# Kernel tuning notes

Measured on AMD Instinct MI355X. Metric: run time of the kernel, lower is better.

Reference implementation:

```python
import jax, jax.numpy as jnp
import numpy as np

K_BINS = 8192
HIDDEN = 2048
SQRT2 = 1.4142135623730951
LEAKY_SLOPE = 0.01
TMIN = 1e-10


def setup_inputs() -> dict:
    key = jax.random.key(0)
    k0, k1, k2 = jax.random.split(key, 3)
    D = 2 * K_BINS  # mu length so that cat([mu, t]) has 2K+1 features
    # positive mu keeps mu ** (gamma - 1/(1-gamma)) (a fractional power) finite
    mu = jax.random.uniform(k0, (D,), jnp.float32, 0.1, 1.0)
    t = jnp.array([0.5], jnp.float32)
    gamma = jnp.array([0.5], jnp.float32)  # 1/(1-gamma) = 2 -> integral exponent
    W1 = jax.random.normal(k1, (D + 1, HIDDEN), jnp.float32) * (1.0 / np.sqrt(D + 1))
    b1 = jnp.zeros((HIDDEN,), jnp.float32)
    W2 = jax.random.normal(k2, (HIDDEN, D), jnp.float32) * (1.0 / np.sqrt(HIDDEN))
    b2 = jnp.zeros((D,), jnp.float32)
    return {"mu": mu, "t": t, "gamma": gamma, "W1": W1, "b1": b1,
            "W2": W2, "b2": b2, "K": K_BINS}


def reference(mu, t, gamma, W1, b1, W2, b2, K):
    g = gamma[0]
    # --- NN(cat([mu, t])) -> (mu_epsilon, ln_sigma_epsilon), each [K] ---
    inp = jnp.concatenate([mu, t])                      # [2K+1]
    h = jax.nn.leaky_relu(inp @ W1 + b1, LEAKY_SLOPE)   # [hidden]
    out = h @ W2 + b2                                   # [2K]
    mu_eps, ln_sig = out[:K], out[K:]
    # --- mu_x / sigma_x (t < tmin branch folded in via where) ---
    p_mu = g - 1.0 / (1.0 - g)
    p_eps = 1.0 / (1.0 - g)
    mu_x_nn = jnp.power(mu[:K], p_mu) * jnp.power(mu_eps, p_eps)
    sigma_x_nn = jnp.power(1.0 - g, -0.5) * jnp.exp(0.5 * ln_sig)
    use_nn = t[0] >= TMIN
    mu_x = jnp.where(use_nn, mu_x_nn, jnp.zeros_like(mu_eps))     # [K]
    sigma_x = jnp.where(use_nn, sigma_x_nn, jnp.ones_like(mu_eps))  # [K]
    # --- vectorized discretised CDF differences over the (D_out, K) grid ---
    kk = jnp.arange(K, dtype=jnp.float32)
    kl = 2.0 * (kk - 1.0) / (K - 1.0)   # left bin edges  [K]
    kr = 2.0 * kk / (K - 1.0)           # right bin edges [K]

    def cdf(x):  # x: [K] edges -> G: [D_out, K]
        z = (x[None, :] - mu_x[:, None]) / (sigma_x[:, None] * SQRT2)
        F = 0.5 * (1.0 + jax.lax.erf(z))
        return jnp.where(x[None, :] <= -1.0, 0.0,
                         jnp.where(x[None, :] >= 1.0, 1.0, F))

    return cdf(kr) - cdf(kl)  # [K, K] per-bin probabilities
```

## Files before the change

### kernel.cpp

```cpp
#include <hip/hip_runtime.h>
#include <math.h>

#define KBINS 8192
#define DDIM  16384
#define HID   2048
#define LASTROW 16384

#define C1 8
#define NCH1 2048
#define C2 8
#define NCH2 256

static constexpr float SQRT2_F  = 1.4142135623730951f;
static constexpr float INVSQ2PI = 0.3989422804014327f;

__device__ __forceinline__ float fast_erff(float x) {
    float ax = fabsf(x);
    float t  = 1.0f / fmaf(0.3275911f, ax, 1.0f);
    float p  = t * (0.254829592f +
               t * (-0.284496736f +
               t * (1.421413741f +
               t * (-1.453152027f +
               t * 1.061405429f))));
    float r = 1.0f - p * __expf(-ax * ax);
    return copysignf(r, x);
}

__global__ void __launch_bounds__(256)
mv1_partial(const float* __restrict__ mu, const float* __restrict__ W1,
            float* __restrict__ part1) {
    __shared__ float a_s[C1];
    int r0 = blockIdx.x * C1;
    if (threadIdx.x < C1) a_s[threadIdx.x] = mu[r0 + threadIdx.x];
    __syncthreads();
    int c0 = threadIdx.x * 4;
    const float* wp = W1 + (size_t)r0 * HID;
    float4 acc0 = {0.f, 0.f, 0.f, 0.f};
    float4 acc1 = {0.f, 0.f, 0.f, 0.f};
#pragma unroll
    for (int k = 0; k < C1; ++k) {
        float a = a_s[k];
        const float4 w0 = *reinterpret_cast<const float4*>(wp + (size_t)k * HID + c0);
        const float4 w1 = *reinterpret_cast<const float4*>(wp + (size_t)k * HID + c0 + 1024);
        acc0.x += a * w0.x; acc0.y += a * w0.y; acc0.z += a * w0.z; acc0.w += a * w0.w;
        acc1.x += a * w1.x; acc1.y += a * w1.y; acc1.z += a * w1.z; acc1.w += a * w1.w;
    }
    float* pp = part1 + (size_t)blockIdx.x * HID;
    *reinterpret_cast<float4*>(pp + c0)        = acc0;
    *reinterpret_cast<float4*>(pp + c0 + 1024) = acc1;
}

__global__ void __launch_bounds__(256)
h_reduce(const float* __restrict__ part1, const float* __restrict__ b1,
         const float* __restrict__ W1, const float* __restrict__ t,
         float* __restrict__ h) {
    __shared__ float red[16][17];
    int col_l = threadIdx.x & 15;
    int sub   = threadIdx.x >> 4;
    int c0    = blockIdx.x * 16;
    float s = 0.f;
    const float* p = part1 + c0 + col_l;
#pragma unroll 8
    for (int m = 0; m < 128; ++m)
        s += p[(size_t)(sub + (m << 4)) * HID];
    red[sub][col_l] = s;
    __syncthreads();
    if (threadIdx.x < 16) {
        int c = c0 + threadIdx.x;
        float v = b1[c] + t[0] * W1[(size_t)LASTROW * HID + c];
#pragma unroll
        for (int q = 0; q < 16; ++q) v += red[q][threadIdx.x];
        h[c] = (v >= 0.f) ? v : 0.01f * v;
    }
}

__global__ void __launch_bounds__(256)
mv2_partial(const float* __restrict__ h, const float* __restrict__ W2,
            float* __restrict__ part2) {
    __shared__ float hs[C2];
    int r0    = blockIdx.y * C2;
    int cbase = blockIdx.x * 2048;
    if (threadIdx.x < C2) hs[threadIdx.x] = h[r0 + threadIdx.x];
    __syncthreads();
    int c0 = cbase + threadIdx.x * 4;
    const float* wp = W2 + (size_t)r0 * DDIM;
    float4 acc0 = {0.f, 0.f, 0.f, 0.f};
    float4 acc1 = {0.f, 0.f, 0.f, 0.f};
#pragma unroll
    for (int k = 0; k < C2; ++k) {
        float a = hs[k];
        const float4 w0 = *reinterpret_cast<const float4*>(wp + (size_t)k * DDIM + c0);
        const float4 w1 = *reinterpret_cast<const float4*>(wp + (size_t)k * DDIM + c0 + 1024);
        acc0.x += a * w0.x; acc0.y += a * w0.y; acc0.z += a * w0.z; acc0.w += a * w0.w;
        acc1.x += a * w1.x; acc1.y += a * w1.y; acc1.z += a * w1.z; acc1.w += a * w1.w;
    }
    float* pp = part2 + (size_t)blockIdx.y * DDIM;
    *reinterpret_cast<float4*>(pp + c0)        = acc0;
    *reinterpret_cast<float4*>(pp + c0 + 1024) = acc1;
}

__global__ void __launch_bounds__(256)
scalars(const float* __restrict__ part2, const float* __restrict__ b2,
        const float* __restrict__ mu, const float* __restrict__ t,
        const float* __restrict__ gamma,
        float* __restrict__ mu_x, float* __restrict__ sigma_x) {
    __shared__ float red0[8][32];
    __shared__ float red1[8][32];
    int col_l = threadIdx.x & 31;
    int sub   = threadIdx.x >> 5;
    int c     = blockIdx.x * 32 + col_l;
    float s0 = 0.f, s1 = 0.f;
    const float* p0 = part2 + c;
    const float* p1 = part2 + c + KBINS;
#pragma unroll 8
    for (int m = 0; m < 32; ++m) {
        size_t off = (size_t)(sub + (m << 3)) * DDIM;
        s0 += p0[off];
        s1 += p1[off];
    }
    red0[sub][col_l] = s0;
    red1[sub][col_l] = s1;
    __syncthreads();
    if (threadIdx.x < 32) {
        int cc = blockIdx.x * 32 + threadIdx.x;
        float v0 = b2[cc];
        float v1 = b2[cc + KBINS];
#pragma unroll
        for (int p = 0; p < 8; ++p) { v0 += red0[p][threadIdx.x]; v1 += red1[p][threadIdx.x]; }
        float g  = gamma[0];
        float pe = 1.0f / (1.0f - g);
        float pm = g - pe;
        bool use_nn = (t[0] >= 1e-10f);
        float mx = powf(mu[cc], pm) * powf(v0, pe);
        float sx = powf(1.0f - g, -0.5f) * expf(0.5f * v1);
        mu_x[cc]    = use_nn ? mx : 0.0f;
        sigma_x[cc] = use_nn ? sx : 1.0f;
    }
}

__global__ void __launch_bounds__(256)
cdf_row(const float* __restrict__ mu_x, const float* __restrict__ sigma_x,
        float* __restrict__ out) {
    int tid = threadIdx.x;
    for (int rr = 0; rr < 2; ++rr) {
        int i = blockIdx.x * 2 + rr;
        float m    = mu_x[i];
        float invs = 1.0f / sigma_x[i];
        const float sc = 2.0f / 8191.0f;
        float A    = sc * invs;
        float B    = (-1.0f / 8191.0f - m) * invs;
        float coef = INVSQ2PI * A;
        float* orow = out + (size_t)i * KBINS;
#pragma unroll
        for (int it = 0; it < 8; ++it) {
            int j0 = it * 1024 + tid * 4;
            float4 r;
            if (j0 < 4096) {
                float u0 = fmaf((float)j0, A, B);
                float u1 = u0 + A;
                float u2 = u1 + A;
                float u3 = u2 + A;
                r.x = coef * __expf(-0.5f * u0 * u0);
                r.y = coef * __expf(-0.5f * u1 * u1);
                r.z = coef * __expf(-0.5f * u2 * u2);
                r.w = coef * __expf(-0.5f * u3 * u3);
            } else if (j0 == 4096) {
                float z = (8190.0f / 8191.0f - m) * invs * (1.0f / SQRT2_F);
                r.x = 0.5f * (1.0f - fast_erff(z));
                r.y = r.z = r.w = 0.f;
            } else {
                r.x = r.y = r.z = r.w = 0.f;
            }
            *reinterpret_cast<float4*>(orow + j0) = r;
        }
    }
}

extern "C" void kernel_launch(void* const* d_in, const int* in_sizes, int n_in,
                              void* d_out, int out_size, void* d_ws, size_t ws_size,
                              hipStream_t stream) {
    const float* mu    = (const float*)d_in[0];
    const float* t     = (const float*)d_in[1];
    const float* gamma = (const float*)d_in[2];
    const float* W1    = (const float*)d_in[3];
    const float* b1    = (const float*)d_in[4];
    const float* W2    = (const float*)d_in[5];
    const float* b2    = (const float*)d_in[6];
    float* out = (float*)d_out;

    float* ws    = (float*)d_ws;
    float* part1 = ws;
    float* h     = part1 + (size_t)NCH1 * HID;
    float* part2 = h + HID;
    float* mu_x  = part2 + (size_t)NCH2 * DDIM;
    float* sig_x = mu_x + KBINS;

    mv1_partial<<<dim3(NCH1),     dim3(256), 0, stream>>>(mu, W1, part1);
    h_reduce   <<<dim3(128),      dim3(256), 0, stream>>>(part1, b1, W1, t, h);
    mv2_partial<<<dim3(8, NCH2),  dim3(256), 0, stream>>>(h, W2, part2);
    scalars    <<<dim3(256),      dim3(256), 0, stream>>>(part2, b2, mu, t, gamma, mu_x, sig_x);
    cdf_row    <<<dim3(4096),     dim3(256), 0, stream>>>(mu_x, sig_x, out);
}
```

Measured before the change: 138.2 us.

## Fuse second matvec, scalar computation and CDF row writing into one kernel

Replaces the mv2_partial, scalars and cdf_row kernels with one fused kernel. Each of 256 blocks computes the 32 mu/ln_sigma pairs it needs through a strided column dot product over W2, derives the per-row constants in shared memory, then writes its 32 output rows. This removes the 16 MB part2 partial-sum round trip and two launches. In exchange it uses only 256 blocks, reads W2 with uncoalesced per-row strided loads, and the output writes now follow the matvec inside each block. h_reduce is also reshaped to 256 blocks of 8 columns.

```diff
diff --git a/kernel.cpp b/kernel.cpp
--- a/kernel.cpp
+++ b/kernel.cpp
@@ -8,8 +8,6 @@
 
 #define C1 8
 #define NCH1 2048
-#define C2 8
-#define NCH2 256
 
 static constexpr float SQRT2_F  = 1.4142135623730951f;
 static constexpr float INVSQ2PI = 0.3989422804014327f;
@@ -54,103 +52,86 @@
 h_reduce(const float* __restrict__ part1, const float* __restrict__ b1,
          const float* __restrict__ W1, const float* __restrict__ t,
          float* __restrict__ h) {
-    __shared__ float red[16][17];
-    int col_l = threadIdx.x & 15;
-    int sub   = threadIdx.x >> 4;
-    int c0    = blockIdx.x * 16;
+    __shared__ float red[32][9];
+    int col_l = threadIdx.x & 7;
+    int sub   = threadIdx.x >> 3;
+    int c0    = blockIdx.x * 8;
     float s = 0.f;
     const float* p = part1 + c0 + col_l;
 #pragma unroll 8
-    for (int m = 0; m < 128; ++m)
-        s += p[(size_t)(sub + (m << 4)) * HID];
+    for (int m = 0; m < 64; ++m)
+        s += p[(size_t)(sub + (m << 5)) * HID];
     red[sub][col_l] = s;
     __syncthreads();
-    if (threadIdx.x < 16) {
+    if (threadIdx.x < 8) {
         int c = c0 + threadIdx.x;
         float v = b1[c] + t[0] * W1[(size_t)LASTROW * HID + c];
 #pragma unroll
-        for (int q = 0; q < 16; ++q) v += red[q][threadIdx.x];
+        for (int q = 0; q < 32; ++q) v += red[q][threadIdx.x];
         h[c] = (v >= 0.f) ? v : 0.01f * v;
     }
 }
 
 __global__ void __launch_bounds__(256)
-mv2_partial(const float* __restrict__ h, const float* __restrict__ W2,
-            float* __restrict__ part2) {
-    __shared__ float hs[C2];
-    int r0    = blockIdx.y * C2;
-    int cbase = blockIdx.x * 2048;
-    if (threadIdx.x < C2) hs[threadIdx.x] = h[r0 + threadIdx.x];
+fused_out(const float* __restrict__ h, const float* __restrict__ W2,
+          const float* __restrict__ b2, const float* __restrict__ mu,
+          const float* __restrict__ t, const float* __restrict__ gamma,
+          float* __restrict__ out) {
+    __shared__ float hs[HID];
+    __shared__ float red[4][64];
+    __shared__ float s01[2][32];
+    __shared__ float sA[32], sB[32], sCf[32], sEr[32];
+    const int tid = threadIdx.x;
+    const int i0  = blockIdx.x * 32;
+
+    for (int q = tid; q < HID; q += 256) hs[q] = h[q];
     __syncthreads();
-    int c0 = cbase + threadIdx.x * 4;
-    const float* wp = W2 + (size_t)r0 * DDIM;
-    float4 acc0 = {0.f, 0.f, 0.f, 0.f};
-    float4 acc1 = {0.f, 0.f, 0.f, 0.f};
-#pragma unroll
-    for (int k = 0; k < C2; ++k) {
-        float a = hs[k];
-        const float4 w0 = *reinterpret_cast<const float4*>(wp + (size_t)k * DDIM + c0);
-        const float4 w1 = *reinterpret_cast<const float4*>(wp + (size_t)k * DDIM + c0 + 1024);
-        acc0.x += a * w0.x; acc0.y += a * w0.y; acc0.z += a * w0.z; acc0.w += a * w0.w;
-        acc1.x += a * w1.x; acc1.y += a * w1.y; acc1.z += a * w1.z; acc1.w += a * w1.w;
+
+    {
+        int col_l = tid & 63;
+        int chunk = tid >> 6;
+        int c = i0 + (col_l & 31) + (col_l >> 5) * KBINS;
+        const float* wp = W2 + c;
+        int rbeg = chunk * 512;
+        float s = 0.f;
+#pragma unroll 16
+        for (int r = rbeg; r < rbeg + 512; ++r)
+            s += hs[r] * wp[(size_t)r * DDIM];
+        red[chunk][col_l] = s;
     }
-    float* pp = part2 + (size_t)blockIdx.y * DDIM;
-    *reinterpret_cast<float4*>(pp + c0)        = acc0;
-    *reinterpret_cast<float4*>(pp + c0 + 1024) = acc1;
-}
-
-__global__ void __launch_bounds__(256)
-scalars(const float* __restrict__ part2, const float* __restrict__ b2,
-        const float* __restrict__ mu, const float* __restrict__ t,
-        const float* __restrict__ gamma,
-        float* __restrict__ mu_x, float* __restrict__ sigma_x) {
-    __shared__ float red0[8][32];
-    __shared__ float red1[8][32];
-    int col_l = threadIdx.x & 31;
-    int sub   = threadIdx.x >> 5;
-    int c     = blockIdx.x * 32 + col_l;
-    float s0 = 0.f, s1 = 0.f;
-    const float* p0 = part2 + c;
-    const float* p1 = part2 + c + KBINS;
-#pragma unroll 8
-    for (int m = 0; m < 32; ++m) {
-        size_t off = (size_t)(sub + (m << 3)) * DDIM;
-        s0 += p0[off];
-        s1 += p1[off];
+    __syncthreads();
+    if (tid < 64) {
+        int cl = tid & 31, hf = tid >> 5;
+        float v = b2[i0 + cl + hf * KBINS]
+                + red[0][tid] + red[1][tid] + red[2][tid] + red[3][tid];
+        s01[hf][cl] = v;
     }
-    red0[sub][col_l] = s0;
-    red1[sub][col_l] = s1;
     __syncthreads();
-    if (threadIdx.x < 32) {
-        int cc = blockIdx.x * 32 + threadIdx.x;
-        float v0 = b2[cc];
-        float v1 = b2[cc + KBINS];
-#pragma unroll
-        for (int p = 0; p < 8; ++p) { v0 += red0[p][threadIdx.x]; v1 += red1[p][threadIdx.x]; }
+    if (tid < 32) {
+        float s0 = s01[0][tid];
+        float s1 = s01[1][tid];
         float g  = gamma[0];
         float pe = 1.0f / (1.0f - g);
         float pm = g - pe;
         bool use_nn = (t[0] >= 1e-10f);
-        float mx = powf(mu[cc], pm) * powf(v0, pe);
-        float sx = powf(1.0f - g, -0.5f) * expf(0.5f * v1);
-        mu_x[cc]    = use_nn ? mx : 0.0f;
-        sigma_x[cc] = use_nn ? sx : 1.0f;
+        float mval = use_nn ? powf(mu[i0 + tid], pm) * powf(s0, pe) : 0.0f;
+        float invs = use_nn ? powf(1.0f - g, 0.5f) * expf(-0.5f * s1) : 1.0f;
+        const float sc = 2.0f / 8191.0f;
+        float A = sc * invs;
+        sA[tid]  = A;
+        sB[tid]  = (-1.0f / 8191.0f - mval) * invs;
+        sCf[tid] = INVSQ2PI * A;
+        float z = (8190.0f / 8191.0f - mval) * invs * (1.0f / SQRT2_F);
+        sEr[tid] = 0.5f * (1.0f - fast_erff(z));
     }
-}
+    __syncthreads();
 
-__global__ void __launch_bounds__(256)
-cdf_row(const float* __restrict__ mu_x, const float* __restrict__ sigma_x,
-        float* __restrict__ out) {
-    int tid = threadIdx.x;
-    for (int rr = 0; rr < 2; ++rr) {
-        int i = blockIdx.x * 2 + rr;
-        float m    = mu_x[i];
-        float invs = 1.0f / sigma_x[i];
-        const float sc = 2.0f / 8191.0f;
-        float A    = sc * invs;
-        float B    = (-1.0f / 8191.0f - m) * invs;
-        float coef = INVSQ2PI * A;
-        float* orow = out + (size_t)i * KBINS;
+    for (int rr = 0; rr < 32; ++rr) {
+        float A    = sA[rr];
+        float B    = sB[rr];
+        float coef = sCf[rr];
+        float er   = sEr[rr];
+        float* orow = out + (size_t)(i0 + rr) * KBINS;
 #pragma unroll
         for (int it = 0; it < 8; ++it) {
             int j0 = it * 1024 + tid * 4;
@@ -165,8 +146,7 @@
                 r.z = coef * __expf(-0.5f * u2 * u2);
                 r.w = coef * __expf(-0.5f * u3 * u3);
             } else if (j0 == 4096) {
-                float z = (8190.0f / 8191.0f - m) * invs * (1.0f / SQRT2_F);
-                r.x = 0.5f * (1.0f - fast_erff(z));
+                r.x = er;
                 r.y = r.z = r.w = 0.f;
             } else {
                 r.x = r.y = r.z = r.w = 0.f;
@@ -191,13 +171,8 @@
     float* ws    = (float*)d_ws;
     float* part1 = ws;
     float* h     = part1 + (size_t)NCH1 * HID;
-    float* part2 = h + HID;
-    float* mu_x  = part2 + (size_t)NCH2 * DDIM;
-    float* sig_x = mu_x + KBINS;
 
-    mv1_partial<<<dim3(NCH1),     dim3(256), 0, stream>>>(mu, W1, part1);
-    h_reduce   <<<dim3(128),      dim3(256), 0, stream>>>(part1, b1, W1, t, h);
-    mv2_partial<<<dim3(8, NCH2),  dim3(256), 0, stream>>>(h, W2, part2);
-    scalars    <<<dim3(256),      dim3(256), 0, stream>>>(part2, b2, mu, t, gamma, mu_x, sig_x);
-    cdf_row    <<<dim3(4096),     dim3(256), 0, stream>>>(mu_x, sig_x, out);
+    mv1_partial<<<dim3(NCH1), dim3(256), 0, stream>>>(mu, W1, part1);
+    h_reduce   <<<dim3(256),  dim3(256), 0, stream>>>(part1, b1, W1, t, h);
+    fused_out  <<<dim3(256),  dim3(256), 0, stream>>>(h, W2, b2, mu, t, gamma, out);
 }
```

Result: no change. 138.6 us (+0.3%).
